# Performance work log

Measured on AMD Instinct MI355X. Metric: run time of the kernel, lower is better.

## Reference

```python
import jax, jax.numpy as jnp
import numpy as np

DT = 1.0 / 200.0  # imu_freq = 200
EPS = 1e-8

def _skew(v):  # [B,3] -> [B,3,3]
    x, y, z = v[:, 0], v[:, 1], v[:, 2]
    zero = jnp.zeros_like(x)
    return jnp.stack([zero, -z, y, z, zero, -x, -y, x, zero], axis=-1).reshape(-1, 3, 3)

def _axis_angle_to_R(w, dt):
    # Rodrigues: R = I + sin(th) K + (1-cos(th)) K^2, th = ||w||*dt
    n = jnp.linalg.norm(w, axis=-1, keepdims=True)          # [B,1]
    theta = n[:, 0] * dt                                     # [B]
    axis = w / (n + EPS)
    K = _skew(axis)
    I = jnp.eye(3, dtype=w.dtype)
    s = jnp.sin(theta)[:, None, None]
    c = jnp.cos(theta)[:, None, None]
    return I + s * K + (1.0 - c) * jnp.einsum('bij,bjk->bik', K, K)

def _R_to_axis_angle(R):
    tr = jnp.trace(R, axis1=-2, axis2=-1)
    angle = jnp.arccos(jnp.clip((tr - 1.0) / 2.0, -1.0 + 1e-7, 1.0 - 1e-7))
    axis = jnp.stack([R[:, 2, 1] - R[:, 1, 2],
                      R[:, 0, 2] - R[:, 2, 0],
                      R[:, 1, 0] - R[:, 0, 1]], axis=-1)
    axis = axis / (2.0 * jnp.sin(angle)[:, None] + EPS)
    return axis, angle

def _aa_to_quat(axis, angle):  # (w, x, y, z)
    h = angle / 2.0
    return jnp.concatenate([jnp.cos(h)[:, None], axis * jnp.sin(h)[:, None]], axis=-1)

def setup_inputs() -> dict:
    key = jax.random.key(0)
    input_seq = jax.random.normal(key, (512, 4096, 6), dtype=jnp.float32)
    return {"input_seq": input_seq}

def reference(input_seq):
    B, T, _ = input_seq.shape
    dtype = input_seq.dtype
    w = jnp.transpose(input_seq[:, :, :3], (1, 0, 2))  # [T,B,3] gyro
    a = jnp.transpose(input_seq[:, :, 3:], (1, 0, 2))  # [T,B,3] accel
    dt = jnp.asarray(DT, dtype)
    dt2_half = dt * dt / 2.0

    dR0 = jnp.broadcast_to(jnp.eye(3, dtype=dtype), (B, 3, 3))
    dv0 = jnp.zeros((B, 3), dtype)
    dp0 = jnp.zeros((B, 3), dtype)

    def step(carry, inp):
        dR, dv, dp = carry
        w_k, a_k = inp
        dR = jnp.einsum('bij,bjk->bik', dR, _axis_angle_to_R(w_k, dt))
        Ra = jnp.einsum('bij,bj->bi', dR, a_k)
        dv = dv + Ra * dt
        dp = dp + dv * dt + Ra * dt2_half  # uses already-updated dv, as in torch code
        axis, angle = _R_to_axis_angle(dR)
        q = _aa_to_quat(axis, angle)
        return (dR, dv, dp), (dp, dv, q)

    _, (ps, vs, qs) = jax.lax.scan(step, (dR0, dv0, dp0), (w, a))
    ps = jnp.transpose(ps, (1, 0, 2))  # [B,T,3]
    vs = jnp.transpose(vs, (1, 0, 2))  # [B,T,3]
    qs = jnp.transpose(qs, (1, 0, 2))  # [B,T,4]
    return jnp.concatenate([input_seq, ps, qs, vs], axis=2)  # [B,T,16]
```

## Files before the change

kernel.cpp:

```cpp
#include <hip/hip_runtime.h>
#include <math.h>

#define T_LEN 4096
#define CHUNK 8
#define NTHR  512
#define NWAVE (NTHR / 64)

typedef float f32x4 __attribute__((ext_vector_type(4)));

__device__ __forceinline__ void make_A(float wx, float wy, float wz, float* A) {
    const float dt  = 1.0f / 200.0f;
    const float dt2 = dt * dt;
    float n2 = wx*wx + wy*wy + wz*wz;
    float t2 = n2 * dt2;
    float s_ = dt  * (1.0f + t2 * (-1.0f/6.0f  + t2 * (1.0f/120.0f)));
    float oc = dt2 * (0.5f + t2 * (-1.0f/24.0f + t2 * (1.0f/720.0f)));
    float xx = wx*wx, yy = wy*wy, zz = wz*wz;
    float xy = wx*wy, xz = wx*wz, yz = wy*wz;
    A[0] = 1.0f - oc*(yy+zz);
    A[1] = -s_*wz + oc*xy;
    A[2] =  s_*wy + oc*xz;
    A[3] =  s_*wz + oc*xy;
    A[4] = 1.0f - oc*(xx+zz);
    A[5] = -s_*wx + oc*yz;
    A[6] = -s_*wy + oc*xz;
    A[7] =  s_*wx + oc*yz;
    A[8] = 1.0f - oc*(xx+yy);
}

__device__ __forceinline__ void matmul3(const float* R, const float* A, float* N) {
#pragma unroll
    for (int i = 0; i < 3; ++i) {
        N[i*3+0] = R[i*3+0]*A[0] + R[i*3+1]*A[3] + R[i*3+2]*A[6];
        N[i*3+1] = R[i*3+0]*A[1] + R[i*3+1]*A[4] + R[i*3+2]*A[7];
        N[i*3+2] = R[i*3+0]*A[2] + R[i*3+1]*A[5] + R[i*3+2]*A[8];
    }
}

__device__ __forceinline__ void step(float* E, float wx, float wy, float wz,
                                     float ax, float ay, float az) {
    const float dt   = 1.0f / 200.0f;
    const float dt2h = dt * dt * 0.5f;
    float A[9], N[9];
    make_A(wx, wy, wz, A);
    matmul3(E, A, N);
#pragma unroll
    for (int i = 0; i < 9; ++i) E[i] = N[i];
    float rax = E[0]*ax + E[1]*ay + E[2]*az;
    float ray = E[3]*ax + E[4]*ay + E[5]*az;
    float raz = E[6]*ax + E[7]*ay + E[8]*az;
    E[9]  += rax*dt; E[10] += ray*dt; E[11] += raz*dt;
    E[12] += E[9]*dt  + rax*dt2h;
    E[13] += E[10]*dt + ray*dt2h;
    E[14] += E[11]*dt + raz*dt2h;
}

__device__ __forceinline__ void compose(const float* __restrict__ L,
                                        float* __restrict__ e, float tauY) {
    float N[9];
    matmul3(L, e, N);
    float b0 = L[9]  + L[0]*e[9] + L[1]*e[10] + L[2]*e[11];
    float b1 = L[10] + L[3]*e[9] + L[4]*e[10] + L[5]*e[11];
    float b2 = L[11] + L[6]*e[9] + L[7]*e[10] + L[8]*e[11];
    float c0 = L[12] + tauY*L[9]  + L[0]*e[12] + L[1]*e[13] + L[2]*e[14];
    float c1 = L[13] + tauY*L[10] + L[3]*e[12] + L[4]*e[13] + L[5]*e[14];
    float c2 = L[14] + tauY*L[11] + L[6]*e[12] + L[7]*e[13] + L[8]*e[14];
#pragma unroll
    for (int i = 0; i < 9; ++i) e[i] = N[i];
    e[9]  = b0; e[10] = b1; e[11] = b2;
    e[12] = c0; e[13] = c1; e[14] = c2;
}

__device__ __forceinline__ float4 quat_of(const float* S) {
    float tr = S[0] + S[4] + S[8];
    float ca = fminf(fmaxf(0.5f * (tr - 1.0f), -1.0f + 1e-7f), 1.0f - 1e-7f);
    float x  = 0.5f * (1.0f + ca);
    float r  = __frsqrt_rn(x);
    float qw = x * r;
    float i4 = 0.25f * r;
    return make_float4(qw, (S[7] - S[5]) * i4,
                           (S[2] - S[6]) * i4,
                           (S[3] - S[1]) * i4);
}

__global__ __launch_bounds__(NTHR, 2)
void preint_kernel(const float* __restrict__ in, float* __restrict__ out) {
    const int b    = blockIdx.x;
    const int t    = threadIdx.x;
    const int lane = t & 63;
    const int w    = t >> 6;
    const float dt = 1.0f / 200.0f;

    const float* bin  = in  + (size_t)b * T_LEN * 6;
    float*       bout = out + (size_t)b * T_LEN * 16;
    const float4* src4 = (const float4*)(bin + (size_t)t * CHUNK * 6);

    __shared__ __align__(16) float4 tile[NTHR * 8];
    float* wtot = (float*)tile;

    float e[15] = {1,0,0, 0,1,0, 0,0,1, 0,0,0, 0,0,0};
#pragma unroll
    for (int pp = 0; pp < CHUNK / 2; ++pp) {
        float4 u0 = src4[pp*3+0];
        float4 u1 = src4[pp*3+1];
        float4 u2 = src4[pp*3+2];
        step(e, u0.x, u0.y, u0.z, u0.w, u1.x, u1.y);
        step(e, u1.z, u1.w, u2.x, u2.y, u2.z, u2.w);
    }

#pragma unroll
    for (int d = 1; d < 64; d <<= 1) {
        float L[15];
#pragma unroll
        for (int i = 0; i < 15; ++i) L[i] = __shfl_up(e[i], d, 64);
        if (lane >= d) compose(L, e, (float)(d * CHUNK) * dt);
    }

    if (lane == 63) {
#pragma unroll
        for (int i = 0; i < 15; ++i) wtot[w*15 + i] = e[i];
    }
    __syncthreads();

    if (w == 0) {
        float s[15] = {1,0,0, 0,1,0, 0,0,1, 0,0,0, 0,0,0};
        if (lane < NWAVE) {
#pragma unroll
            for (int i = 0; i < 15; ++i) s[i] = wtot[lane*15 + i];
        }
#pragma unroll
        for (int d = 1; d < NWAVE; d <<= 1) {
            float L[15];
#pragma unroll
            for (int i = 0; i < 15; ++i) L[i] = __shfl_up(s[i], d, 64);
            if (lane >= d && lane < NWAVE)
                compose(L, s, (float)(d * 64 * CHUNK) * dt);
        }
        if (lane < NWAVE) {
#pragma unroll
            for (int i = 0; i < 15; ++i) wtot[lane*15 + i] = s[i];
        }
    }
    __syncthreads();

    float st[15];
#pragma unroll
    for (int i = 0; i < 15; ++i) st[i] = __shfl_up(e[i], 1, 64);
    if (lane == 0) {
        st[0]=1; st[1]=0; st[2]=0; st[3]=0; st[4]=1; st[5]=0;
        st[6]=0; st[7]=0; st[8]=1; st[9]=0; st[10]=0; st[11]=0;
        st[12]=0; st[13]=0; st[14]=0;
    }
    {
        float P[15] = {1,0,0, 0,1,0, 0,0,1, 0,0,0, 0,0,0};
        if (w > 0) {
#pragma unroll
            for (int i = 0; i < 15; ++i) P[i] = wtot[(w-1)*15 + i];
        }
        compose(P, st, (float)(lane * CHUNK) * dt);
    }
    __syncthreads();

    const float4* src4b;
    {
        unsigned long long pbits = (unsigned long long)src4;
        asm volatile("" : "+v"(pbits) : "v"(st[0]), "v"(st[14]));
        src4b = (const float4*)pbits;
    }
    __builtin_amdgcn_sched_barrier(0);

    float4* wt  = tile + (size_t)w * 512;
    f32x4*  go4 = (f32x4*)bout + (size_t)w * 2048;
    const int swz = lane & 7;

#pragma unroll
    for (int pp = 0; pp < CHUNK / 2; ++pp) {
        float4 u0 = src4b[pp*3+0];
        float4 u1 = src4b[pp*3+1];
        float4 u2 = src4b[pp*3+2];

        step(st, u0.x, u0.y, u0.z, u0.w, u1.x, u1.y);
        {
            float4 q = quat_of(st);
            wt[(lane*8 + 0) ^ swz] = make_float4(u0.x, u0.y, u0.z, u0.w);
            wt[(lane*8 + 1) ^ swz] = make_float4(u1.x, u1.y, st[12], st[13]);
            wt[(lane*8 + 2) ^ swz] = make_float4(st[14], q.x, q.y, q.z);
            wt[(lane*8 + 3) ^ swz] = make_float4(q.w, st[9], st[10], st[11]);
        }

        step(st, u1.z, u1.w, u2.x, u2.y, u2.z, u2.w);
        {
            float4 q = quat_of(st);
            wt[(lane*8 + 4) ^ swz] = make_float4(u1.z, u1.w, u2.x, u2.y);
            wt[(lane*8 + 5) ^ swz] = make_float4(u2.z, u2.w, st[12], st[13]);
            wt[(lane*8 + 6) ^ swz] = make_float4(st[14], q.x, q.y, q.z);
            wt[(lane*8 + 7) ^ swz] = make_float4(q.w, st[9], st[10], st[11]);
        }

        asm volatile("s_waitcnt lgkmcnt(0)" ::: "memory");
        __builtin_amdgcn_sched_barrier(0);

#pragma unroll
        for (int i = 0; i < 8; ++i) {
            int c = i*64 + lane;
            float4 v = wt[c ^ ((c >> 3) & 7)];
            f32x4 vv = { v.x, v.y, v.z, v.w };
            int g = i*256 + (lane >> 3)*32 + pp*8 + (lane & 7);
            __builtin_nontemporal_store(vv, &go4[g]);
        }
        __builtin_amdgcn_sched_barrier(0);
    }
}

extern "C" void kernel_launch(void* const* d_in, const int* in_sizes, int n_in,
                              void* d_out, int out_size, void* d_ws, size_t ws_size,
                              hipStream_t stream) {
    const float* in = (const float*)d_in[0];
    float* out = (float*)d_out;
    const int B = in_sizes[0] / (T_LEN * 6);
    preint_kernel<<<dim3(B), dim3(NTHR), 0, stream>>>(in, out);
}
```

Baseline: 183.0 us.

## Split scan into segment-totals and emit kernels across four segments per batch

Each batch's time sequence is split into four segments handled by separate blocks, with CHUNK reduced from 8 to 2. A first kernel computes per-segment composed totals into workspace, and a second kernel re-scans each segment, prefixes the earlier segment totals, and writes the output. This raises the number of blocks from B to 4B to improve GPU occupancy and parallelism. The cost is reading the input twice, an extra kernel launch, and more scan/compose work per element.

```diff
diff --git a/kernel.cpp b/kernel.cpp
--- a/kernel.cpp
+++ b/kernel.cpp
@@ -2,9 +2,11 @@
 #include <math.h>
 
 #define T_LEN 4096
-#define CHUNK 8
 #define NTHR  512
 #define NWAVE (NTHR / 64)
+#define CHUNK 2
+#define SEG   (NTHR * CHUNK)
+#define NSEG  (T_LEN / SEG)
 
 typedef float f32x4 __attribute__((ext_vector_type(4)));
 
@@ -83,30 +85,81 @@
                            (S[3] - S[1]) * i4);
 }
 
-__global__ __launch_bounds__(NTHR, 2)
-void preint_kernel(const float* __restrict__ in, float* __restrict__ out) {
-    const int b    = blockIdx.x;
+__global__ __launch_bounds__(NTHR)
+void totals_kernel(const float* __restrict__ in, float* __restrict__ ws) {
+    const int g    = blockIdx.x;
+    const int b    = g >> 2;
+    const int s    = g & (NSEG - 1);
     const int t    = threadIdx.x;
     const int lane = t & 63;
     const int w    = t >> 6;
     const float dt = 1.0f / 200.0f;
 
-    const float* bin  = in  + (size_t)b * T_LEN * 6;
-    float*       bout = out + (size_t)b * T_LEN * 16;
-    const float4* src4 = (const float4*)(bin + (size_t)t * CHUNK * 6);
+    const float4* src4 = (const float4*)(in +
+        ((size_t)b * T_LEN + (size_t)s * SEG + (size_t)t * CHUNK) * 6);
+    float4 u0 = src4[0], u1 = src4[1], u2 = src4[2];
+
+    float e[15] = {1,0,0, 0,1,0, 0,0,1, 0,0,0, 0,0,0};
+    step(e, u0.x, u0.y, u0.z, u0.w, u1.x, u1.y);
+    step(e, u1.z, u1.w, u2.x, u2.y, u2.z, u2.w);
+
+#pragma unroll
+    for (int d = 1; d < 64; d <<= 1) {
+        float L[15];
+#pragma unroll
+        for (int i = 0; i < 15; ++i) L[i] = __shfl_up(e[i], d, 64);
+        if (lane >= d) compose(L, e, (float)(d * CHUNK) * dt);
+    }
+
+    __shared__ float wtot[NWAVE * 15];
+    if (lane == 63) {
+#pragma unroll
+        for (int i = 0; i < 15; ++i) wtot[w*15 + i] = e[i];
+    }
+    __syncthreads();
+
+    if (w == 0) {
+        float sv[15] = {1,0,0, 0,1,0, 0,0,1, 0,0,0, 0,0,0};
+        if (lane < NWAVE) {
+#pragma unroll
+            for (int i = 0; i < 15; ++i) sv[i] = wtot[lane*15 + i];
+        }
+#pragma unroll
+        for (int d = 1; d < NWAVE; d <<= 1) {
+            float L[15];
+#pragma unroll
+            for (int i = 0; i < 15; ++i) L[i] = __shfl_up(sv[i], d, 64);
+            if (lane >= d && lane < NWAVE)
+                compose(L, sv, (float)(d * 64 * CHUNK) * dt);
+        }
+        if (lane == NWAVE - 1) {
+#pragma unroll
+            for (int i = 0; i < 15; ++i) ws[(size_t)g * 15 + i] = sv[i];
+        }
+    }
+}
+
+__global__ __launch_bounds__(NTHR, 2)
+void emit_kernel(const float* __restrict__ in, const float* __restrict__ ws,
+                 float* __restrict__ out) {
+    const int g    = blockIdx.x;
+    const int b    = g >> 2;
+    const int s    = g & (NSEG - 1);
+    const int t    = threadIdx.x;
+    const int lane = t & 63;
+    const int w    = t >> 6;
+    const float dt = 1.0f / 200.0f;
+
+    const float4* src4 = (const float4*)(in +
+        ((size_t)b * T_LEN + (size_t)s * SEG + (size_t)t * CHUNK) * 6);
+    float4 u0 = src4[0], u1 = src4[1], u2 = src4[2];
 
     __shared__ __align__(16) float4 tile[NTHR * 8];
     float* wtot = (float*)tile;
 
     float e[15] = {1,0,0, 0,1,0, 0,0,1, 0,0,0, 0,0,0};
-#pragma unroll
-    for (int pp = 0; pp < CHUNK / 2; ++pp) {
-        float4 u0 = src4[pp*3+0];
-        float4 u1 = src4[pp*3+1];
-        float4 u2 = src4[pp*3+2];
-        step(e, u0.x, u0.y, u0.z, u0.w, u1.x, u1.y);
-        step(e, u1.z, u1.w, u2.x, u2.y, u2.z, u2.w);
-    }
+    step(e, u0.x, u0.y, u0.z, u0.w, u1.x, u1.y);
+    step(e, u1.z, u1.w, u2.x, u2.y, u2.z, u2.w);
 
 #pragma unroll
     for (int d = 1; d < 64; d <<= 1) {
@@ -123,22 +176,22 @@
     __syncthreads();
 
     if (w == 0) {
-        float s[15] = {1,0,0, 0,1,0, 0,0,1, 0,0,0, 0,0,0};
+        float sv[15] = {1,0,0, 0,1,0, 0,0,1, 0,0,0, 0,0,0};
         if (lane < NWAVE) {
 #pragma unroll
-            for (int i = 0; i < 15; ++i) s[i] = wtot[lane*15 + i];
+            for (int i = 0; i < 15; ++i) sv[i] = wtot[lane*15 + i];
         }
 #pragma unroll
         for (int d = 1; d < NWAVE; d <<= 1) {
             float L[15];
 #pragma unroll
-            for (int i = 0; i < 15; ++i) L[i] = __shfl_up(s[i], d, 64);
+            for (int i = 0; i < 15; ++i) L[i] = __shfl_up(sv[i], d, 64);
             if (lane >= d && lane < NWAVE)
-                compose(L, s, (float)(d * 64 * CHUNK) * dt);
+                compose(L, sv, (float)(d * 64 * CHUNK) * dt);
         }
         if (lane < NWAVE) {
 #pragma unroll
-            for (int i = 0; i < 15; ++i) wtot[lane*15 + i] = s[i];
+            for (int i = 0; i < 15; ++i) wtot[lane*15 + i] = sv[i];
         }
     }
     __syncthreads();
@@ -161,54 +214,54 @@
     }
     __syncthreads();
 
-    const float4* src4b;
-    {
-        unsigned long long pbits = (unsigned long long)src4;
-        asm volatile("" : "+v"(pbits) : "v"(st[0]), "v"(st[14]));
-        src4b = (const float4*)pbits;
-    }
+    {
+        float P0[15] = {1,0,0, 0,1,0, 0,0,1, 0,0,0, 0,0,0};
+#pragma unroll
+        for (int k = 0; k < NSEG - 1; ++k) {
+            if (k < s) {
+                float tmp[15];
+                const float* Tk = ws + (size_t)(g - s + k) * 15;
+#pragma unroll
+                for (int i = 0; i < 15; ++i) tmp[i] = Tk[i];
+                compose(P0, tmp, (float)SEG * dt);
+#pragma unroll
+                for (int i = 0; i < 15; ++i) P0[i] = tmp[i];
+            }
+        }
+        compose(P0, st, (float)(t * CHUNK) * dt);
+    }
+
+    float4* wt  = tile + (size_t)w * 512;
+    const int swz = lane & 7;
+
+    step(st, u0.x, u0.y, u0.z, u0.w, u1.x, u1.y);
+    {
+        float4 q = quat_of(st);
+        wt[(lane*8 + 0) ^ swz] = make_float4(u0.x, u0.y, u0.z, u0.w);
+        wt[(lane*8 + 1) ^ swz] = make_float4(u1.x, u1.y, st[12], st[13]);
+        wt[(lane*8 + 2) ^ swz] = make_float4(st[14], q.x, q.y, q.z);
+        wt[(lane*8 + 3) ^ swz] = make_float4(q.w, st[9], st[10], st[11]);
+    }
+    step(st, u1.z, u1.w, u2.x, u2.y, u2.z, u2.w);
+    {
+        float4 q = quat_of(st);
+        wt[(lane*8 + 4) ^ swz] = make_float4(u1.z, u1.w, u2.x, u2.y);
+        wt[(lane*8 + 5) ^ swz] = make_float4(u2.z, u2.w, st[12], st[13]);
+        wt[(lane*8 + 6) ^ swz] = make_float4(st[14], q.x, q.y, q.z);
+        wt[(lane*8 + 7) ^ swz] = make_float4(q.w, st[9], st[10], st[11]);
+    }
+
+    asm volatile("s_waitcnt lgkmcnt(0)" ::: "memory");
     __builtin_amdgcn_sched_barrier(0);
 
-    float4* wt  = tile + (size_t)w * 512;
-    f32x4*  go4 = (f32x4*)bout + (size_t)w * 2048;
-    const int swz = lane & 7;
-
-#pragma unroll
-    for (int pp = 0; pp < CHUNK / 2; ++pp) {
-        float4 u0 = src4b[pp*3+0];
-        float4 u1 = src4b[pp*3+1];
-        float4 u2 = src4b[pp*3+2];
-
-        step(st, u0.x, u0.y, u0.z, u0.w, u1.x, u1.y);
-        {
-            float4 q = quat_of(st);
-            wt[(lane*8 + 0) ^ swz] = make_float4(u0.x, u0.y, u0.z, u0.w);
-            wt[(lane*8 + 1) ^ swz] = make_float4(u1.x, u1.y, st[12], st[13]);
-            wt[(lane*8 + 2) ^ swz] = make_float4(st[14], q.x, q.y, q.z);
-            wt[(lane*8 + 3) ^ swz] = make_float4(q.w, st[9], st[10], st[11]);
-        }
-
-        step(st, u1.z, u1.w, u2.x, u2.y, u2.z, u2.w);
-        {
-            float4 q = quat_of(st);
-            wt[(lane*8 + 4) ^ swz] = make_float4(u1.z, u1.w, u2.x, u2.y);
-            wt[(lane*8 + 5) ^ swz] = make_float4(u2.z, u2.w, st[12], st[13]);
-            wt[(lane*8 + 6) ^ swz] = make_float4(st[14], q.x, q.y, q.z);
-            wt[(lane*8 + 7) ^ swz] = make_float4(q.w, st[9], st[10], st[11]);
-        }
-
-        asm volatile("s_waitcnt lgkmcnt(0)" ::: "memory");
-        __builtin_amdgcn_sched_barrier(0);
-
-#pragma unroll
-        for (int i = 0; i < 8; ++i) {
-            int c = i*64 + lane;
-            float4 v = wt[c ^ ((c >> 3) & 7)];
-            f32x4 vv = { v.x, v.y, v.z, v.w };
-            int g = i*256 + (lane >> 3)*32 + pp*8 + (lane & 7);
-            __builtin_nontemporal_store(vv, &go4[g]);
-        }
-        __builtin_amdgcn_sched_barrier(0);
+    f32x4* go4 = (f32x4*)(out + ((size_t)b * T_LEN + (size_t)s * SEG) * 16)
+                 + (size_t)w * 512;
+#pragma unroll
+    for (int i = 0; i < 8; ++i) {
+        int c = i*64 + lane;
+        float4 v = wt[c ^ ((c >> 3) & 7)];
+        f32x4 vv = { v.x, v.y, v.z, v.w };
+        __builtin_nontemporal_store(vv, &go4[c]);
     }
 }
 
@@ -217,6 +270,8 @@
                               hipStream_t stream) {
     const float* in = (const float*)d_in[0];
     float* out = (float*)d_out;
+    float* ws  = (float*)d_ws;
     const int B = in_sizes[0] / (T_LEN * 6);
-    preint_kernel<<<dim3(B), dim3(NTHR), 0, stream>>>(in, out);
-}
+    totals_kernel<<<dim3(B * NSEG), dim3(NTHR), 0, stream>>>(in, ws);
+    emit_kernel<<<dim3(B * NSEG), dim3(NTHR), 0, stream>>>(in, ws, out);
+}
```

Measured after the change: 221.4 us. 21.0% more time.
